# Performance work log

Hardware: AMD Instinct MI355X
Metric: run time of the kernel (lower is better)

The kernel has to match this reference:

```python
import jax, jax.numpy as jnp
import numpy as np

B, T, S, DENC = 32, 256, 1600, 1024
V, EMB, PRE, LSTMU, A, F, K = 1000, 512, 256, 1024, 128, 32, 31


def _lstm_step(x, h, c, W, U, b):
    z = x @ W + h @ U + b
    i, f, g, o = jnp.split(z, 4, axis=-1)
    c2 = jax.nn.sigmoid(f) * c + jax.nn.sigmoid(i) * jnp.tanh(g)
    h2 = jax.nn.sigmoid(o) * jnp.tanh(c2)
    return h2, c2


def setup_inputs() -> dict:
    key = jax.random.key(0)
    ks = jax.random.split(key, 32)
    sc = 0.02
    d = {}
    d['tokens'] = jax.random.randint(ks[0], (B, T), 0, V, dtype=jnp.int32)
    d['memory'] = jax.random.normal(ks[1], (B, S, DENC), dtype=jnp.float32)
    d['memory_length'] = jax.random.randint(ks[2], (B,), S // 2, S, dtype=jnp.int32)
    d['emb'] = sc * jax.random.normal(ks[3], (V, EMB), jnp.float32)
    d['Wp1'] = sc * jax.random.normal(ks[4], (EMB, PRE), jnp.float32)
    d['bp1'] = jnp.zeros((PRE,), jnp.float32)
    d['Wp2'] = sc * jax.random.normal(ks[5], (PRE, PRE), jnp.float32)
    d['bp2'] = jnp.zeros((PRE,), jnp.float32)
    d['Wq'] = sc * jax.random.normal(ks[6], (LSTMU, A), jnp.float32)
    d['Wmem'] = sc * jax.random.normal(ks[7], (DENC, A), jnp.float32)
    d['conv_k'] = sc * jax.random.normal(ks[8], (K, 1, F), jnp.float32)
    d['Wloc'] = sc * jax.random.normal(ks[9], (F, A), jnp.float32)
    d['Wv'] = sc * jax.random.normal(ks[10], (A, 1), jnp.float32)
    d['bv'] = jnp.zeros((1,), jnp.float32)
    d['Wa'] = sc * jax.random.normal(ks[11], (PRE + DENC, 4 * LSTMU), jnp.float32)
    d['Ua'] = sc * jax.random.normal(ks[12], (LSTMU, 4 * LSTMU), jnp.float32)
    d['ba'] = jnp.zeros((4 * LSTMU,), jnp.float32)
    d['W0'] = sc * jax.random.normal(ks[13], (LSTMU + DENC, 4 * LSTMU), jnp.float32)
    d['U0'] = sc * jax.random.normal(ks[14], (LSTMU, 4 * LSTMU), jnp.float32)
    d['b0'] = jnp.zeros((4 * LSTMU,), jnp.float32)
    d['W1'] = sc * jax.random.normal(ks[15], (LSTMU, 4 * LSTMU), jnp.float32)
    d['U1'] = sc * jax.random.normal(ks[16], (LSTMU, 4 * LSTMU), jnp.float32)
    d['b1'] = jnp.zeros((4 * LSTMU,), jnp.float32)
    d['Wc'] = sc * jax.random.normal(ks[17], (LSTMU + DENC, V), jnp.float32)
    d['bc'] = jnp.zeros((V,), jnp.float32)
    d['Ws'] = sc * jax.random.normal(ks[18], (LSTMU + V, 1), jnp.float32)
    d['bs'] = jnp.zeros((1,), jnp.float32)
    return d


def reference(tokens, memory, memory_length, emb, Wp1, bp1, Wp2, bp2, Wq, Wmem,
              conv_k, Wloc, Wv, bv, Wa, Ua, ba, W0, U0, b0, W1, U1, b1,
              Wc, bc, Ws, bs):
    Sdim = memory.shape[1]
    keys = jnp.einsum('bsd,da->bsa', memory, Wmem)            # [B,S,A], computed once
    mask = jnp.arange(Sdim)[None, :] < memory_length[:, None]  # [B,S]
    neg = jnp.float32(-1e9)

    def step(carry, tok):
        h_a, c_a, h0, c0, h1, c1, ctx, ast = carry
        x = emb[tok]                                           # [B,EMB]
        p = jax.nn.relu(x @ Wp1 + bp1)
        p = jax.nn.relu(p @ Wp2 + bp2)                         # prenet (dropout omitted)
        h_a, c_a = _lstm_step(jnp.concatenate([p, ctx], -1), h_a, c_a, Wa, Ua, ba)
        pq = h_a @ Wq                                          # [B,A]
        f = jax.lax.conv_general_dilated(ast[:, :, None], conv_k, (1,), 'SAME',
                                         dimension_numbers=('NWC', 'WIO', 'NWC'))  # [B,S,F]
        ploc = f @ Wloc                                        # [B,S,A]
        e = jnp.squeeze(jnp.tanh(keys + pq[:, None, :] + ploc) @ Wv, -1) + bv  # [B,S]
        e = jnp.where(mask, e, neg)
        al = jax.nn.softmax(e, axis=-1)
        ast = ast + al                                         # cumulative alignments
        ctx = jnp.einsum('bs,bsd->bd', al, memory)
        h0, c0 = _lstm_step(jnp.concatenate([h_a, ctx], -1), h0, c0, W0, U0, b0)
        h1, c1 = _lstm_step(h0, h1, c1, W1, U1, b1)
        proj = jnp.concatenate([h1, ctx], -1)
        cls = proj @ Wc + bc                                   # [B,V]
        stp = jnp.concatenate([h1, cls], -1) @ Ws + bs         # [B,1]
        return (h_a, c_a, h0, c0, h1, c1, ctx, ast), (cls, stp)

    Bz = tokens.shape[0]
    z = lambda n: jnp.zeros((Bz, n), jnp.float32)
    init = (z(LSTMU), z(LSTMU), z(LSTMU), z(LSTMU), z(LSTMU), z(LSTMU),
            z(memory.shape[2]), z(Sdim))
    _, (cls, stp) = jax.lax.scan(step, init, tokens.T)         # stacked [T,B,...]
    return jnp.transpose(cls, (1, 0, 2)), jnp.transpose(stp, (1, 0, 2))
```

## Files before the change

### kernel.cpp

```cpp
#include <hip/hip_runtime.h>

#define BB 32
#define TT 256
#define SS 1600
#define DE 1024
#define VV 1000
#define EM 512
#define PR 256
#define LU 1024
#define AA 128
#define FF 32
#define KK 31
#define KSC 32
#define KSTEP 16
#define NBUF 3

typedef __attribute__((ext_vector_type(8))) short short8;
typedef __attribute__((ext_vector_type(4))) float f32x4;

__device__ __forceinline__ float bf2f(ushort u) {
  unsigned int x = ((unsigned int)u) << 16;
  return __builtin_bit_cast(float, x);
}
__device__ __forceinline__ ushort f2bf(float f) {
  unsigned int x = __builtin_bit_cast(unsigned int, f);
  return (ushort)((x + 0x7FFFu + ((x >> 16) & 1u)) >> 16);
}
__device__ __forceinline__ void gload16(const void* g, void* l) {
  __builtin_amdgcn_global_load_lds(
      (const __attribute__((address_space(1))) void*)g,
      (__attribute__((address_space(3))) void*)l, 16, 0, 0);
}
__device__ __forceinline__ float ftanh(float x) {
  float e = __expf(2.f * x);
  return 1.f - 2.f / (e + 1.f);
}
__device__ __forceinline__ float fsig(float x) {
  return 1.f / (1.f + __expf(-x));
}


__global__ __launch_bounds__(256) void conv_mem(const float* __restrict__ in,
                                                ushort* __restrict__ out, int n4)
{
  int i = blockIdx.x * 256 + threadIdx.x;
  if (i < n4) {
    float4 v = *(const float4*)(in + (size_t)i * 4);
    ushort4 o;
    o.x = f2bf(v.x); o.y = f2bf(v.y); o.z = f2bf(v.z); o.w = f2bf(v.w);
    *(ushort4*)(out + (size_t)i * 4) = o;
  }
}

__global__ __launch_bounds__(256) void pack_wu(const float* __restrict__ Wm,
    const float* __restrict__ Um, int lenW, int ktot, ushort* __restrict__ out, int nS)
{
  int bid = blockIdx.x;
  int kg = bid & 3, S = (bid >> 2) % nS, jb = (bid >> 2) / nS;
  int t = threadIdx.x;
  int c = t >> 1, e4 = (t & 1) * 4;
  int kbase = S * 32 + kg * 8 + e4;
  int j = jb * 128 + c;
  ushort* op = out + ((size_t)(jb * nS + S) * 4 + kg) * 1024 + c * 8 + e4;
#pragma unroll
  for (int i = 0; i < 4; i++) {
    int k = kbase + i;
    float v = 0.f;
    if (k < lenW)      v = Wm[(size_t)k * 4096 + j];
    else if (k < ktot) v = Um[(size_t)(k - lenW) * 4096 + j];
    op[i] = f2bf(v);
  }
}

__global__ __launch_bounds__(256) void keys_kernel(const float* __restrict__ mem,
                                                   const float* __restrict__ Wmem,
                                                   float* __restrict__ keys)
{
  int stile = blockIdx.x;
  int b = blockIdx.y;
  int t = threadIdx.x;
  __shared__ float Xt[8 * 1032];
  const float* mp = mem + ((size_t)b * SS + (size_t)stile * 8) * DE;
  for (int li = t; li < 8 * 256; li += 256) {
    int row = li >> 8, c4 = li & 255;
    float4 v = *(const float4*)(mp + row * DE + c4 * 4);
    *(float4*)(Xt + row * 1032 + c4 * 4) = v;
  }
  __syncthreads();
  int sl = t >> 5, u = t & 31;
  float acc[4] = {0.f, 0.f, 0.f, 0.f};
  for (int k = 0; k < DE; k++) {
    float x = Xt[sl * 1032 + k];
    const float* wr = Wmem + k * AA;
#pragma unroll
    for (int jj = 0; jj < 4; jj++) acc[jj] += x * wr[u + 32 * jj];
  }
  float* kp = keys + ((size_t)b * SS + (size_t)stile * 8 + sl) * AA;
#pragma unroll
  for (int jj = 0; jj < 4; jj++) kp[u + 32 * jj] = acc[jj];
}

__global__ void mconv_kernel(const float* __restrict__ ck, const float* __restrict__ Wloc,
                             float* __restrict__ M)
{
  int a = threadIdx.x;
  int k = blockIdx.x;
  float acc = 0.f;
  for (int c = 0; c < FF; c++) acc += ck[k * FF + c] * Wloc[c * AA + a];
  M[k * AA + a] = acc;
}

__global__ __launch_bounds__(256) void prenet_all(const int* __restrict__ tokens,
    const float* __restrict__ emb, const float* __restrict__ Wp1, const float* __restrict__ bp1,
    const float* __restrict__ Wp2, const float* __restrict__ bp2, float* __restrict__ P)
{
  int tstep = blockIdx.x;
  int bh = blockIdx.y;
  int t = threadIdx.x;
  __shared__ float X[16 * 512];
  __shared__ float P1[16 * 256];
  for (int li = t; li < 16 * 128; li += 256) {
    int bb = li >> 7, c4 = li & 127;
    int tok = tokens[(bh * 16 + bb) * TT + tstep];
    *(float4*)(X + bb * 512 + c4 * 4) = *(const float4*)(emb + (size_t)tok * EM + c4 * 4);
  }
  __syncthreads();
  int j = t;
  float acc[16];
#pragma unroll
  for (int i = 0; i < 16; i++) acc[i] = 0.f;
  for (int k = 0; k < EM; k++) {
    float w = Wp1[k * PR + j];
#pragma unroll
    for (int i = 0; i < 16; i++) acc[i] += X[i * 512 + k] * w;
  }
#pragma unroll
  for (int i = 0; i < 16; i++) P1[i * 256 + j] = fmaxf(acc[i] + bp1[j], 0.f);
  __syncthreads();
#pragma unroll
  for (int i = 0; i < 16; i++) acc[i] = 0.f;
  for (int k = 0; k < PR; k++) {
    float w = Wp2[k * PR + j];
#pragma unroll
    for (int i = 0; i < 16; i++) acc[i] += P1[i * 256 + k] * w;
  }
  float* outp = P + (size_t)tstep * BB * PR + (size_t)bh * 16 * PR;
#pragma unroll
  for (int i = 0; i < 16; i++) outp[i * PR + j] = fmaxf(acc[i] + bp2[j], 0.f);
}


__device__ void gemm_dev(int jb, int kc,
    const float* x0, int len0, const float* x1, int len1, const float* x2, int len2,
    const ushort* WUP, int nS, int chunk, float* zp, char* ldsraw)
{
  ushort* wlT = (ushort*)ldsraw;
  ushort* xl  = (ushort*)(ldsraw + 49152);
  const int t = threadIdx.x;
  const int lane = t & 63;
  const int wv = __builtin_amdgcn_readfirstlane(t >> 6);
  const int PADK = chunk + 8;
  const int nst = chunk >> 6;
  const int k0 = kc * chunk;
  const int S0 = k0 >> 5;
  const size_t jbS = (size_t)jb * nS;
  const int lenW01 = len0 + len1;
  const int ktot = lenW01 + len2;

  auto stage = [&](int s) {
    int buf = s % 3;
    int Sb = S0 + s * 2;
#pragma unroll
    for (int sub = 0; sub < 4; sub++) {
      int inst = wv * 4 + sub;
      const ushort* src = WUP + (jbS + Sb + (inst >> 3)) * 4096
                        + (size_t)(((inst & 7) * 64 + lane) * 8);
      ushort* dst = wlT + buf * 8192 + inst * 512;
      gload16(src, dst);
    }
  };

  stage(0);
  stage(1);

  for (int b = 0; b < 32; b++) {
    for (int kk = t; kk < chunk; kk += 256) {
      int k = k0 + kk;
      float val = 0.f;
      if (k < ktot) {
        const float* xp; int str; int off;
        if (k < len0)        { xp = x0; str = len0; off = k; }
        else if (k < lenW01) { xp = x1; str = len1; off = k - len0; }
        else                 { xp = x2; str = len2; off = k - lenW01; }
        val = xp[(size_t)b * str + off];
      }
      xl[b * PADK + kk] = f2bf(val);
    }
  }
  __syncthreads();

  f32x4 acc[2][2];
#pragma unroll
  for (int mt = 0; mt < 2; mt++)
#pragma unroll
    for (int nt = 0; nt < 2; nt++)
#pragma unroll
      for (int r = 0; r < 4; r++) acc[mt][nt][r] = 0.f;

  const int lane15 = lane & 15, kg = lane >> 4;

  for (int s = 0; s < nst; s++) {
    if (s + 2 < nst) stage(s + 2);
    int ahead = nst - 1 - s; if (ahead > 2) ahead = 2;
    if (ahead == 2)      asm volatile("s_waitcnt vmcnt(8)");
    else if (ahead == 1) asm volatile("s_waitcnt vmcnt(4)");
    else                 asm volatile("s_waitcnt vmcnt(0)");
    __builtin_amdgcn_s_barrier();
    __builtin_amdgcn_sched_barrier(0);
    const ushort* bb = wlT + (s % 3) * 8192 + kg * 1024 + (wv * 32 + lane15) * 8;
    const ushort* ab = xl + lane15 * PADK + s * 64 + kg * 8;
#pragma unroll
    for (int kh = 0; kh < 2; kh++) {
      short8 b0 = *(const short8*)(bb + kh * 4096);
      short8 b1 = *(const short8*)(bb + kh * 4096 + 128);
      short8 a0 = *(const short8*)(ab + kh * 32);
      short8 a1 = *(const short8*)(ab + kh * 32 + 16 * PADK);
      acc[0][0] = __builtin_amdgcn_mfma_f32_16x16x32_bf16(a0, b0, acc[0][0], 0, 0, 0);
      acc[0][1] = __builtin_amdgcn_mfma_f32_16x16x32_bf16(a0, b1, acc[0][1], 0, 0, 0);
      acc[1][0] = __builtin_amdgcn_mfma_f32_16x16x32_bf16(a1, b0, acc[1][0], 0, 0, 0);
      acc[1][1] = __builtin_amdgcn_mfma_f32_16x16x32_bf16(a1, b1, acc[1][1], 0, 0, 0);
    }
    asm volatile("s_waitcnt lgkmcnt(0)");
    __builtin_amdgcn_sched_barrier(0);
    __builtin_amdgcn_s_barrier();
  }

  int colb = jb * 128 + wv * 32 + lane15;
  int rowb = kg * 4;
#pragma unroll
  for (int mt = 0; mt < 2; mt++)
#pragma unroll
    for (int nt = 0; nt < 2; nt++)
#pragma unroll
      for (int r = 0; r < 4; r++) {
        int b = mt * 16 + rowb + r;
        zp[((size_t)kc * BB + b) * 4096 + colb + nt * 16] = acc[mt][nt][r];
      }
}

__device__ void finish_dev(int b, int q, const float* zpart, const float* bias,
    float* h, float* c, const float* Wq, float* pqp, char* ldsraw)
{
  float* sh  = (float*)ldsraw;
  float* sh2 = sh + 256;
  int t = threadIdx.x;
  int j = q * 256 + t;
  float zi = bias[j], zf = bias[LU + j], zg = bias[2 * LU + j], zo = bias[3 * LU + j];
#pragma unroll
  for (int kc = 0; kc < 8; kc++) {
    const float* zpt = zpart + ((size_t)kc * BB + b) * 4096;
    zi += zpt[j]; zf += zpt[LU + j]; zg += zpt[2 * LU + j]; zo += zpt[3 * LU + j];
  }
  float cn = fsig(zf) * c[b * LU + j] + fsig(zi) * ftanh(zg);
  float hn = fsig(zo) * ftanh(cn);
  c[b * LU + j] = cn;
  h[b * LU + j] = hn;

  if (pqp) {
    sh[t] = hn;
    __syncthreads();
    int a = t & 127, half = t >> 7;
    float acc = 0.f;
    const float* wq = Wq + ((size_t)(q * 256 + half * 128)) * AA + a;
#pragma unroll 4
    for (int jj = 0; jj < 128; jj++) acc += sh[half * 128 + jj] * wq[(size_t)jj * AA];
    sh2[t] = acc;
    __syncthreads();
    if (t < 128) pqp[(size_t)q * BB * AA + b * AA + t] = sh2[t] + sh2[t + 128];
  }
}

__device__ void energy_dev(int tile, int b, const float* keys, const float* pqp,
    const float* M, const float* ast, const float* Wv, const float* bv,
    const int* mlen, float* e, char* ldsraw)
{
  int s0 = tile * 128;
  int ml = mlen[b];
  if (s0 >= ml) return;
  float* astT = (float*)ldsraw;
  float* Ml4  = astT + 368;
  float* wvp  = Ml4 + 31 * 132;
  int t = threadIdx.x;
  for (int idx = t; idx < 368; idx += 256) {
    int G = idx >> 3, i = idx & 7;
    int s = s0 + G - 15 + 16 * i;
    astT[idx] = (s >= 0 && s < SS) ? ast[b * SS + s] : 0.f;
  }
  for (int idx = t; idx < KK * AA; idx += 256) {
    int k = idx >> 7, a = idx & 127;
    Ml4[k * 132 + a] = M[idx];
  }
  if (t < 128) wvp[t] = Wv[t];
  else {
    int a = t - 128;
    wvp[128 + a] = pqp[b * AA + a] + pqp[(size_t)BB * AA + b * AA + a]
                 + pqp[(size_t)2 * BB * AA + b * AA + a]
                 + pqp[(size_t)3 * BB * AA + b * AA + a];
  }
  __syncthreads();
  int u = t & 15, g = t >> 4;
  int a0 = u * 8;
  float4 wv0 = *(float4*)&wvp[a0], wv1 = *(float4*)&wvp[a0 + 4];
  float4 pq0 = *(float4*)&wvp[128 + a0], pq1 = *(float4*)&wvp[128 + a0 + 4];
  float arg[8][8];
#pragma unroll
  for (int i = 0; i < 8; i++) {
    int s = s0 + g + 16 * i;
    if (s < SS) {
      const float* kp = keys + ((size_t)b * SS + s) * AA + a0;
      float4 k0 = *(const float4*)kp, k1 = *(const float4*)(kp + 4);
      arg[i][0] = k0.x + pq0.x; arg[i][1] = k0.y + pq0.y;
      arg[i][2] = k0.z + pq0.z; arg[i][3] = k0.w + pq0.w;
      arg[i][4] = k1.x + pq1.x; arg[i][5] = k1.y + pq1.y;
      arg[i][6] = k1.z + pq1.z; arg[i][7] = k1.w + pq1.w;
    } else {
#pragma unroll
      for (int jj = 0; jj < 8; jj++) arg[i][jj] = 0.f;
    }
  }
  for (int k = 0; k < KK; k++) {
    float4 m0 = *(float4*)&Ml4[k * 132 + a0];
    float4 m1 = *(float4*)&Ml4[k * 132 + a0 + 4];
    float4 as0 = *(float4*)&astT[(g + k) * 8];
    float4 as1 = *(float4*)&astT[(g + k) * 8 + 4];
    float asv[8] = {as0.x, as0.y, as0.z, as0.w, as1.x, as1.y, as1.z, as1.w};
#pragma unroll
    for (int i = 0; i < 8; i++) {
      float aw = asv[i];
      arg[i][0] += aw * m0.x; arg[i][1] += aw * m0.y;
      arg[i][2] += aw * m0.z; arg[i][3] += aw * m0.w;
      arg[i][4] += aw * m1.x; arg[i][5] += aw * m1.y;
      arg[i][6] += aw * m1.z; arg[i][7] += aw * m1.w;
    }
  }
  float bvv = bv[0];
#pragma unroll
  for (int i = 0; i < 8; i++) {
    int s = s0 + g + 16 * i;
    float v = ftanh(arg[i][0]) * wv0.x + ftanh(arg[i][1]) * wv0.y
            + ftanh(arg[i][2]) * wv0.z + ftanh(arg[i][3]) * wv0.w
            + ftanh(arg[i][4]) * wv1.x + ftanh(arg[i][5]) * wv1.y
            + ftanh(arg[i][6]) * wv1.z + ftanh(arg[i][7]) * wv1.w;
#pragma unroll
    for (int m = 1; m < 16; m <<= 1) v += __shfl_xor(v, m);
    if (u == 0 && s < SS) e[b * SS + s] = (s < ml) ? (v + bvv) : -1e9f;
  }
}

__device__ void ctxsm_dev(int sc, int b, const float* e, const int* mlen,
    const ushort* mem_bf, float* ast, float* cp, char* ldsraw)
{
  float* red  = (float*)ldsraw;
  float* alsh = red + 4;
  int ml = mlen[b];
  int s0 = sc * 100;
  int cnt = ml - s0; if (cnt > 100) cnt = 100;
  if (cnt <= 0) return;
  int t = threadIdx.x;
  const float* er = e + b * SS;
  float m = -3e38f;
  for (int s = t; s < ml; s += 256) m = fmaxf(m, er[s]);
#pragma unroll
  for (int msk = 1; msk < 64; msk <<= 1) m = fmaxf(m, __shfl_xor(m, msk));
  if ((t & 63) == 0) red[t >> 6] = m;
  __syncthreads();
  m = fmaxf(fmaxf(red[0], red[1]), fmaxf(red[2], red[3]));
  __syncthreads();
  float sum = 0.f;
  for (int s = t; s < ml; s += 256) sum += __expf(er[s] - m);
#pragma unroll
  for (int msk = 1; msk < 64; msk <<= 1) sum += __shfl_xor(sum, msk);
  if ((t & 63) == 0) red[t >> 6] = sum;
  __syncthreads();
  float inv = 1.f / (red[0] + red[1] + red[2] + red[3]);
  if (t < cnt) {
    float a_ = __expf(er[s0 + t] - m) * inv;
    alsh[t] = a_;
    ast[b * SS + s0 + t] += a_;
  }
  __syncthreads();
  float4 acc = make_float4(0.f, 0.f, 0.f, 0.f);
  const ushort* mp = mem_bf + ((size_t)b * SS + s0) * DE + t * 4;
#pragma unroll 4
  for (int i = 0; i < cnt; i++) {
    uint2 v = *(const uint2*)(mp + (size_t)i * DE);
    float a_ = alsh[i];
    acc.x += a_ * bf2f((ushort)(v.x & 0xffff));
    acc.y += a_ * bf2f((ushort)(v.x >> 16));
    acc.z += a_ * bf2f((ushort)(v.y & 0xffff));
    acc.w += a_ * bf2f((ushort)(v.y >> 16));
  }
  *(float4*)&cp[((size_t)sc * BB + b) * DE + t * 4] = acc;
}

__device__ void ctxred_dev(int b, const float* cp, const int* mlen, float* ctx)
{
  int t = threadIdx.x;
  int nsc = (mlen[b] + 99) / 100; if (nsc > 16) nsc = 16;
  float4 acc = make_float4(0.f, 0.f, 0.f, 0.f);
  for (int sc = 0; sc < nsc; sc++) {
    float4 v = *(const float4*)&cp[((size_t)sc * BB + b) * DE + t * 4];
    acc.x += v.x; acc.y += v.y; acc.z += v.z; acc.w += v.w;
  }
  *(float4*)&ctx[b * DE + t * 4] = acc;
}

__device__ void gemv_dev(int jb, int kc,
    const float* x0, int len0, const float* x1, int len1, const float* x2, int len2,
    const float* Wmat, const float* Umat, int N, int chunk, float* zp, char* ldsraw)
{
  float* wl = (float*)ldsraw;
  float* xl = wl + NBUF * KSTEP * 256;
  int t = threadIdx.x;
  int lane = t & 63;
  int wv = __builtin_amdgcn_readfirstlane(t >> 6);
  int lenW = len0 + len1;
  int k0 = kc * chunk;
  int nst = chunk >> 4;
  int colbase = jb * 256 + lane * 4;
  bool jok = (colbase + 4 <= N);

#pragma unroll
  for (int bi = 0; bi < 8; bi++) {
    int b = wv * 8 + bi;
    for (int kk = lane; kk < chunk; kk += 64) {
      int k = k0 + kk;
      const float* xp; int str; int off;
      if (k < len0)      { xp = x0; str = len0; off = k; }
      else if (k < lenW) { xp = x1; str = len1; off = k - len0; }
      else               { xp = x2; str = len2; off = k - lenW; }
      xl[b * 256 + kk] = xp[(size_t)b * str + off];
    }
  }
  __syncthreads();

  auto stage = [&](int s) {
    int buf = s % NBUF;
    int rbase = k0 + s * KSTEP + wv * 4;
#pragma unroll
    for (int rr = 0; rr < 4; rr++) {
      int r = rbase + rr;
      const float* src = (r < lenW) ? (Wmat + (size_t)r * N + colbase)
                                    : (Umat + (size_t)(r - lenW) * N + colbase);
      float* dst = &wl[(buf * KSTEP + (wv * 4 + rr)) * 256];
      if (jok) gload16(src, dst);
    }
  };

  if (nst > 0) stage(0);
  if (nst > 1) stage(1);

  float acc[8][4];
#pragma unroll
  for (int bi = 0; bi < 8; bi++)
    for (int cc = 0; cc < 4; cc++) acc[bi][cc] = 0.f;

  for (int s = 0; s < nst; s++) {
    if (s + 2 < nst) stage(s + 2);
    int ahead = nst - 1 - s; if (ahead > 2) ahead = 2;
    if (ahead == 2)      asm volatile("s_waitcnt vmcnt(8)");
    else if (ahead == 1) asm volatile("s_waitcnt vmcnt(4)");
    else                 asm volatile("s_waitcnt vmcnt(0)");
    __builtin_amdgcn_s_barrier();
    __builtin_amdgcn_sched_barrier(0);
    const float* wb = &wl[(s % NBUF) * KSTEP * 256];
    int xoff = s * KSTEP;
#pragma unroll
    for (int k4 = 0; k4 < 4; k4++) {
      float4 xv[8];
#pragma unroll
      for (int bi = 0; bi < 8; bi++)
        xv[bi] = *(const float4*)&xl[(wv * 8 + bi) * 256 + xoff + k4 * 4];
#pragma unroll
      for (int kk = 0; kk < 4; kk++) {
        float4 w = *(const float4*)&wb[(k4 * 4 + kk) * 256 + lane * 4];
#pragma unroll
        for (int bi = 0; bi < 8; bi++) {
          float xs = (&xv[bi].x)[kk];
          acc[bi][0] += xs * w.x; acc[bi][1] += xs * w.y;
          acc[bi][2] += xs * w.z; acc[bi][3] += xs * w.w;
        }
      }
    }
    asm volatile("s_waitcnt lgkmcnt(0)");
    __builtin_amdgcn_sched_barrier(0);
    __builtin_amdgcn_s_barrier();
  }

  if (jok) {
#pragma unroll
    for (int bi = 0; bi < 8; bi++) {
      int b = wv * 8 + bi;
      *(float4*)&zp[((size_t)kc * BB + b) * N + colbase] =
          make_float4(acc[bi][0], acc[bi][1], acc[bi][2], acc[bi][3]);
    }
  }
}

__device__ void cls_dev(int b, const float* zpc, const float* bc, const float* h1,
                        const float* Ws, const float* bs, float* out, int ts, char* ldsraw)
{
  float* red = (float*)ldsraw;
  int t = threadIdx.x;
  float sacc = 0.f;
  for (int k = t; k < LU; k += 256) sacc += h1[b * LU + k] * Ws[k];
  float* orow = out + (size_t)b * TT * VV + (size_t)ts * VV;
  for (int v = t; v < VV; v += 256) {
    float acc = bc[v];
#pragma unroll
    for (int kc = 0; kc < KSC; kc++) acc += zpc[((size_t)kc * BB + b) * VV + v];
    orow[v] = acc;
    sacc += acc * Ws[LU + v];
  }
#pragma unroll
  for (int msk = 1; msk < 64; msk <<= 1) sacc += __shfl_xor(sacc, msk);
  if ((t & 63) == 0) red[t >> 6] = sacc;
  __syncthreads();
  if (t == 0) out[(size_t)BB * TT * VV + (size_t)b * TT + ts] =
      red[0] + red[1] + red[2] + red[3] + bs[0];
}


__global__ __launch_bounds__(256) void k_gg(
    int nA, const float* ax0, int al0, const float* ax1, int al1,
    const float* ax2, int al2, const ushort* aW, int anS, int achunk, float* azp,
    int nB, const float* bx0, int bl0, const float* bx1, int bl1,
    const float* bx2, int bl2, const ushort* bW, int bnS, int bchunk, float* bzp,
    const float* zpc, const float* bc, const float* h1c,
    const float* Ws, const float* bs, float* out, int ts)
{
  __shared__ alignas(16) char lds[74240];
  int bid = blockIdx.x;
  if (bid < nA + nB) {
    bool fst = bid < nA;
    int l = fst ? bid : bid - nA;
    gemm_dev(l >> 3, l & 7,
             fst ? ax0 : bx0, fst ? al0 : bl0,
             fst ? ax1 : bx1, fst ? al1 : bl1,
             fst ? ax2 : bx2, fst ? al2 : bl2,
             fst ? aW : bW, fst ? anS : bnS, fst ? achunk : bchunk,
             fst ? azp : bzp, lds);
  } else {
    cls_dev(bid - nA - nB, zpc, bc, h1c, Ws, bs, out, ts, lds);
  }
}

__global__ __launch_bounds__(256) void k_ff(
    int n1, const float* z1, const float* bi1, float* h1_, float* c1_,
    const float* Wq1, float* pqp1,
    const float* z2, const float* bi2, float* h2_, float* c2_,
    const float* Wq2, float* pqp2)
{
  __shared__ alignas(16) char lds[4096];
  int bid = blockIdx.x;
  bool fst = bid < n1;
  int l = fst ? bid : bid - n1;
  finish_dev(l >> 2, l & 3,
             fst ? z1 : z2, fst ? bi1 : bi2, fst ? h1_ : h2_, fst ? c1_ : c2_,
             fst ? Wq1 : Wq2, fst ? pqp1 : pqp2, lds);
}

__global__ __launch_bounds__(256) void k_ge(
    int n1, const float* gx0, int gl0, const float* gx1, int gl1,
    const float* gx2, int gl2, const ushort* gW, int gnS, int gchunk, float* gzp,
    const float* keys, const float* pqp, const float* M, const float* ast,
    const float* Wv, const float* bv, const int* mlen, float* e)
{
  __shared__ alignas(16) char lds[74240];
  int bid = blockIdx.x;
  if (bid < n1) {
    gemm_dev(bid >> 3, bid & 7, gx0, gl0, gx1, gl1, gx2, gl2,
             gW, gnS, gchunk, gzp, lds);
  } else {
    int l = bid - n1;
    energy_dev(l / 32, l % 32, keys, pqp, M, ast, Wv, bv, mlen, e, lds);
  }
}

__global__ __launch_bounds__(256) void k_fs(
    int n1, const float* z1, const float* bi1, float* h1_, float* c1_,
    const float* e, const int* mlen, const ushort* membf, float* ast, float* cp)
{
  __shared__ alignas(16) char lds[4096];
  int bid = blockIdx.x;
  if (bid < n1) {
    finish_dev(bid >> 2, bid & 3, z1, bi1, h1_, c1_, nullptr, nullptr, lds);
  } else {
    int l = bid - n1;
    ctxsm_dev(l >> 5, l & 31, e, mlen, membf, ast, cp, lds);
  }
}

__global__ __launch_bounds__(256) void k_gr(
    int n1, const float* vx0, int vl0, const float* vx1, int vl1,
    const float* vx2, int vl2, const float* Wm, const float* Um, int N, int vchunk,
    float* vzp, const float* cp, const int* mlen, float* ctxout)
{
  __shared__ alignas(16) char lds[81920];
  int bid = blockIdx.x;
  if (bid < n1) {
    gemv_dev(bid >> 5, bid & 31, vx0, vl0, vx1, vl1, vx2, vl2,
             Wm, Um, N, vchunk, vzp, lds);
  } else {
    ctxred_dev(bid - n1, cp, mlen, ctxout);
  }
}


extern "C" void kernel_launch(void* const* d_in, const int* in_sizes, int n_in,
                              void* d_out, int out_size, void* d_ws, size_t ws_size,
                              hipStream_t stream)
{
  const int*   tokens = (const int*)  d_in[0];
  const float* memory = (const float*)d_in[1];
  const int*   mlen   = (const int*)  d_in[2];
  const float* emb    = (const float*)d_in[3];
  const float* Wp1    = (const float*)d_in[4];
  const float* bp1    = (const float*)d_in[5];
  const float* Wp2    = (const float*)d_in[6];
  const float* bp2    = (const float*)d_in[7];
  const float* Wq     = (const float*)d_in[8];
  const float* Wmem   = (const float*)d_in[9];
  const float* convk  = (const float*)d_in[10];
  const float* Wloc   = (const float*)d_in[11];
  const float* Wv     = (const float*)d_in[12];
  const float* bv     = (const float*)d_in[13];
  const float* Wa     = (const float*)d_in[14];
  const float* Ua     = (const float*)d_in[15];
  const float* ba     = (const float*)d_in[16];
  const float* W0     = (const float*)d_in[17];
  const float* U0     = (const float*)d_in[18];
  const float* b0     = (const float*)d_in[19];
  const float* W1     = (const float*)d_in[20];
  const float* U1     = (const float*)d_in[21];
  const float* b1     = (const float*)d_in[22];
  const float* Wc     = (const float*)d_in[23];
  const float* bc     = (const float*)d_in[24];
  const float* Ws     = (const float*)d_in[25];
  const float* bs     = (const float*)d_in[26];
  float* out = (float*)d_out;
  float* ws = (float*)d_ws;

  size_t o = 0;
  float* keys  = ws + o;  o += (size_t)BB * SS * AA;
  float* Mv    = ws + o;  o += 4096;
  float* P_all = ws + o;  o += (size_t)TT * BB * PR;
  float* st    = ws + o;
  float* h_a = st;
  float* c_a = h_a + BB * LU;
  float* h0  = c_a + BB * LU;
  float* c0  = h0 + BB * LU;
  float* h1  = c0 + BB * LU;
  float* c1  = h1 + BB * LU;
  float* ctx2 = c1 + BB * LU;
  float* ast = ctx2 + 2 * BB * DE;
  size_t stcount = (size_t)6 * BB * LU + (size_t)2 * BB * DE + (size_t)BB * SS;
  o += stcount;
  float* pqp  = ws + o;  o += (size_t)4 * BB * AA;
  float* ebuf = ws + o;  o += (size_t)BB * SS;
  float* zpA  = ws + o;  o += (size_t)8 * BB * 4096;
  float* zp0  = ws + o;  o += (size_t)8 * BB * 4096;
  float* zp1  = ws + o;  o += (size_t)8 * BB * 4096;
  float* zpc  = ws + o;  o += (size_t)KSC * BB * VV;
  float* cp   = ws + o;  o += (size_t)16 * BB * DE;
  ushort* membf = (ushort*)(ws + o);  o += (size_t)BB * SS * DE / 2;
  ushort* WUPa  = (ushort*)(ws + o);  o += (size_t)2560 * 4096 / 2;
  ushort* WUP0  = (ushort*)(ws + o);  o += (size_t)3072 * 4096 / 2;
  ushort* WUP1  = (ushort*)(ws + o);  o += (size_t)2048 * 4096 / 2;

  hipMemsetAsync(st, 0, stcount * sizeof(float), stream);
  conv_mem<<<(BB * SS * DE / 4 + 255) / 256, 256, 0, stream>>>(memory, membf,
                                                               BB * SS * DE / 4);
  pack_wu<<<32 * 80 * 4, 256, 0, stream>>>(Wa, Ua, PR + DE, 2304, WUPa, 80);
  pack_wu<<<32 * 96 * 4, 256, 0, stream>>>(W0, U0, LU + DE, 3072, WUP0, 96);
  pack_wu<<<32 * 64 * 4, 256, 0, stream>>>(W1, U1, LU, 2048, WUP1, 64);
  keys_kernel<<<dim3(200, BB), 256, 0, stream>>>(memory, Wmem, keys);
  mconv_kernel<<<KK, AA, 0, stream>>>(convk, Wloc, Mv);
  prenet_all<<<dim3(TT, 2), 256, 0, stream>>>(tokens, emb, Wp1, bp1, Wp2, bp2, P_all);

  auto ctx_at = [&](int t) { return ctx2 + (size_t)(t & 1) * BB * DE; };

  k_gg<<<256, 256, 0, stream>>>(
      0, P_all, PR, ctx_at(1), DE, h_a, LU, WUPa, 80, 320, zpA,
      256, P_all, PR, ctx_at(1), DE, h_a, LU, WUPa, 80, 320, zpA,
      zpc, bc, h1, Ws, bs, out, 0);
  k_ff<<<128, 256, 0, stream>>>(
      128, zpA, ba, h_a, c_a, Wq, pqp,
      zpA, ba, h_a, c_a, Wq, pqp);
  k_ge<<<416, 256, 0, stream>>>(
      0, h_a, LU, ctx_at(0), DE, h0, LU, WUP0, 96, 384, zp0,
      keys, pqp, Mv, ast, Wv, bv, mlen, ebuf);
  k_fs<<<512, 256, 0, stream>>>(
      0, zp0, b0, h0, c0,
      ebuf, mlen, membf, ast, cp);
  k_gr<<<32, 256, 0, stream>>>(
      0, h1, LU, ctx_at(0), DE, h1, 0, Wc, Wc, VV, 64, zpc,
      cp, mlen, ctx_at(0));

  for (int t = 0; t < TT - 1; t++) {
    int ncls = (t > 0) ? 32 : 0;
    k_gg<<<512 + ncls, 256, 0, stream>>>(
        256, h_a, LU, ctx_at(t), DE, h0, LU, WUP0, 96, 384, zp0,
        256, P_all + (size_t)(t + 1) * BB * PR, PR, ctx_at(t), DE, h_a, LU,
        WUPa, 80, 320, zpA,
        zpc, bc, h1, Ws, bs, out, t - 1);
    k_ff<<<256, 256, 0, stream>>>(
        128, zp0, b0, h0, c0, nullptr, nullptr,
        zpA, ba, h_a, c_a, Wq, pqp);
    k_ge<<<672, 256, 0, stream>>>(
        256, h0, LU, h1, LU, h0, 0, WUP1, 64, 256, zp1,
        keys, pqp, Mv, ast, Wv, bv, mlen, ebuf);
    k_fs<<<640, 256, 0, stream>>>(
        128, zp1, b1, h1, c1,
        ebuf, mlen, membf, ast, cp);
    k_gr<<<160, 256, 0, stream>>>(
        128, h1, LU, ctx_at(t), DE, h1, 0, Wc, Wc, VV, 64, zpc,
        cp, mlen, ctx_at(t + 1));
  }

  {
    int t = TT - 1;
    k_gg<<<256 + 32, 256, 0, stream>>>(
        256, h_a, LU, ctx_at(t), DE, h0, LU, WUP0, 96, 384, zp0,
        0, P_all, PR, ctx_at(t), DE, h_a, LU, WUPa, 80, 320, zpA,
        zpc, bc, h1, Ws, bs, out, t - 1);
    k_ff<<<128, 256, 0, stream>>>(
        128, zp0, b0, h0, c0, nullptr, nullptr,
        zp0, b0, h0, c0, nullptr, nullptr);
    k_ge<<<256, 256, 0, stream>>>(
        256, h0, LU, h1, LU, h0, 0, WUP1, 64, 256, zp1,
        keys, pqp, Mv, ast, Wv, bv, mlen, ebuf);
    k_fs<<<128, 256, 0, stream>>>(
        128, zp1, b1, h1, c1,
        ebuf, mlen, membf, ast, cp);
    k_gr<<<128, 256, 0, stream>>>(
        128, h1, LU, ctx_at(t), DE, h1, 0, Wc, Wc, VV, 64, zpc,
        cp, mlen, ctx_at(t + 1));
    k_gg<<<32, 256, 0, stream>>>(
        0, h_a, LU, ctx_at(t), DE, h0, LU, WUP0, 96, 384, zp0,
        0, P_all, PR, ctx_at(t), DE, h_a, LU, WUPa, 80, 320, zpA,
        zpc, bc, h1, Ws, bs, out, t);
  }
}
```

Before: 27.42 ms.

## Reduce per-step kernel launches by atomic context reduction and restaged pipeline

The per-timestep schedule is restructured from five kernels into four. The context partial-sum buffer and its separate reduction pass are replaced by atomicAdd accumulation into a context buffer that a co-scheduled block zeroes in advance. The classifier GEMV is deferred one step and fused into the LSTM-finish kernel, and the classifier/stop output is fused into the energy kernel. The GEMV pipeline also drops from triple to double buffering. The goal is to cut launch and serialization overhead in the 256-step recurrence, at the cost of atomic contention, non-deterministic summation order, and a shallower prefetch depth.

```diff
diff --git a/kernel.cpp b/kernel.cpp
--- a/kernel.cpp
+++ b/kernel.cpp
@@ -357,14 +357,14 @@
   }
 }
 
-__device__ void ctxsm_dev(int sc, int b, const float* e, const int* mlen,
-    const ushort* mem_bf, float* ast, float* cp, char* ldsraw)
+__device__ void ctxsm_atomic_dev(int sc, int b, const float* e, const int* mlen,
+    const ushort* mem_bf, float* ast, float* ctx, char* ldsraw)
 {
   float* red  = (float*)ldsraw;
   float* alsh = red + 4;
   int ml = mlen[b];
-  int s0 = sc * 100;
-  int cnt = ml - s0; if (cnt > 100) cnt = 100;
+  int s0 = sc * 200;
+  int cnt = ml - s0; if (cnt > 200) cnt = 200;
   if (cnt <= 0) return;
   int t = threadIdx.x;
   const float* er = e + b * SS;
@@ -400,27 +400,19 @@
     acc.z += a_ * bf2f((ushort)(v.y & 0xffff));
     acc.w += a_ * bf2f((ushort)(v.y >> 16));
   }
-  *(float4*)&cp[((size_t)sc * BB + b) * DE + t * 4] = acc;
-}
-
-__device__ void ctxred_dev(int b, const float* cp, const int* mlen, float* ctx)
-{
-  int t = threadIdx.x;
-  int nsc = (mlen[b] + 99) / 100; if (nsc > 16) nsc = 16;
-  float4 acc = make_float4(0.f, 0.f, 0.f, 0.f);
-  for (int sc = 0; sc < nsc; sc++) {
-    float4 v = *(const float4*)&cp[((size_t)sc * BB + b) * DE + t * 4];
-    acc.x += v.x; acc.y += v.y; acc.z += v.z; acc.w += v.w;
-  }
-  *(float4*)&ctx[b * DE + t * 4] = acc;
-}
-
-__device__ void gemv_dev(int jb, int kc,
+  float* cpx = ctx + b * DE + t * 4;
+  atomicAdd(cpx + 0, acc.x);
+  atomicAdd(cpx + 1, acc.y);
+  atomicAdd(cpx + 2, acc.z);
+  atomicAdd(cpx + 3, acc.w);
+}
+
+__device__ void gemv2_dev(int jb, int kc,
     const float* x0, int len0, const float* x1, int len1, const float* x2, int len2,
     const float* Wmat, const float* Umat, int N, int chunk, float* zp, char* ldsraw)
 {
   float* wl = (float*)ldsraw;
-  float* xl = wl + NBUF * KSTEP * 256;
+  float* xl = wl + 2 * KSTEP * 256;
   int t = threadIdx.x;
   int lane = t & 63;
   int wv = __builtin_amdgcn_readfirstlane(t >> 6);
@@ -445,7 +437,7 @@
   __syncthreads();
 
   auto stage = [&](int s) {
-    int buf = s % NBUF;
+    int buf = s & 1;
     int rbase = k0 + s * KSTEP + wv * 4;
 #pragma unroll
     for (int rr = 0; rr < 4; rr++) {
@@ -458,7 +450,6 @@
   };
 
   if (nst > 0) stage(0);
-  if (nst > 1) stage(1);
 
   float acc[8][4];
 #pragma unroll
@@ -466,14 +457,11 @@
     for (int cc = 0; cc < 4; cc++) acc[bi][cc] = 0.f;
 
   for (int s = 0; s < nst; s++) {
-    if (s + 2 < nst) stage(s + 2);
-    int ahead = nst - 1 - s; if (ahead > 2) ahead = 2;
-    if (ahead == 2)      asm volatile("s_waitcnt vmcnt(8)");
-    else if (ahead == 1) asm volatile("s_waitcnt vmcnt(4)");
-    else                 asm volatile("s_waitcnt vmcnt(0)");
+    if (s + 1 < nst) { stage(s + 1); asm volatile("s_waitcnt vmcnt(4)"); }
+    else             { asm volatile("s_waitcnt vmcnt(0)"); }
     __builtin_amdgcn_s_barrier();
     __builtin_amdgcn_sched_barrier(0);
-    const float* wb = &wl[(s % NBUF) * KSTEP * 256];
+    const float* wb = &wl[(s & 1) * KSTEP * 256];
     int xoff = s * KSTEP;
 #pragma unroll
     for (int k4 = 0; k4 < 4; k4++) {
@@ -535,84 +523,79 @@
     int nA, const float* ax0, int al0, const float* ax1, int al1,
     const float* ax2, int al2, const ushort* aW, int anS, int achunk, float* azp,
     int nB, const float* bx0, int bl0, const float* bx1, int bl1,
-    const float* bx2, int bl2, const ushort* bW, int bnS, int bchunk, float* bzp,
-    const float* zpc, const float* bc, const float* h1c,
-    const float* Ws, const float* bs, float* out, int ts)
+    const float* bx2, int bl2, const ushort* bW, int bnS, int bchunk, float* bzp)
 {
   __shared__ alignas(16) char lds[74240];
   int bid = blockIdx.x;
-  if (bid < nA + nB) {
-    bool fst = bid < nA;
-    int l = fst ? bid : bid - nA;
-    gemm_dev(l >> 3, l & 7,
-             fst ? ax0 : bx0, fst ? al0 : bl0,
-             fst ? ax1 : bx1, fst ? al1 : bl1,
-             fst ? ax2 : bx2, fst ? al2 : bl2,
-             fst ? aW : bW, fst ? anS : bnS, fst ? achunk : bchunk,
-             fst ? azp : bzp, lds);
+  bool fst = bid < nA;
+  int l = fst ? bid : bid - nA;
+  gemm_dev(l >> 3, l & 7,
+           fst ? ax0 : bx0, fst ? al0 : bl0,
+           fst ? ax1 : bx1, fst ? al1 : bl1,
+           fst ? ax2 : bx2, fst ? al2 : bl2,
+           fst ? aW : bW, fst ? anS : bnS, fst ? achunk : bchunk,
+           fst ? azp : bzp, lds);
+}
+
+__global__ __launch_bounds__(256) void k_ffg(
+    int nf0, const float* z0, const float* bi0, float* h0p, float* c0p,
+    int nf1, const float* z1, const float* bi1, float* h1p, float* c1p,
+    const float* Wq, float* pqp,
+    int ng, const float* vx0, int vl0, const float* vx1, int vl1,
+    const float* vx2, int vl2, const float* Wm, const float* Um, int N, int vchunk,
+    float* vzp)
+{
+  __shared__ alignas(16) char lds[65536];
+  int bid = blockIdx.x;
+  if (bid < nf0) {
+    finish_dev(bid >> 2, bid & 3, z0, bi0, h0p, c0p, nullptr, nullptr, lds);
+  } else if (bid < nf0 + nf1) {
+    int l = bid - nf0;
+    finish_dev(l >> 2, l & 3, z1, bi1, h1p, c1p, Wq, pqp, lds);
   } else {
-    cls_dev(bid - nA - nB, zpc, bc, h1c, Ws, bs, out, ts, lds);
-  }
-}
-
-__global__ __launch_bounds__(256) void k_ff(
-    int n1, const float* z1, const float* bi1, float* h1_, float* c1_,
-    const float* Wq1, float* pqp1,
-    const float* z2, const float* bi2, float* h2_, float* c2_,
-    const float* Wq2, float* pqp2)
-{
-  __shared__ alignas(16) char lds[4096];
-  int bid = blockIdx.x;
-  bool fst = bid < n1;
-  int l = fst ? bid : bid - n1;
-  finish_dev(l >> 2, l & 3,
-             fst ? z1 : z2, fst ? bi1 : bi2, fst ? h1_ : h2_, fst ? c1_ : c2_,
-             fst ? Wq1 : Wq2, fst ? pqp1 : pqp2, lds);
-}
-
-__global__ __launch_bounds__(256) void k_ge(
-    int n1, const float* gx0, int gl0, const float* gx1, int gl1,
+    int l = bid - nf0 - nf1;
+    gemv2_dev(l >> 5, l & 31, vx0, vl0, vx1, vl1, vx2, vl2,
+              Wm, Um, N, vchunk, vzp, lds);
+  }
+}
+
+__global__ __launch_bounds__(256) void k_gec(
+    int nG, const float* gx0, int gl0, const float* gx1, int gl1,
     const float* gx2, int gl2, const ushort* gW, int gnS, int gchunk, float* gzp,
-    const float* keys, const float* pqp, const float* M, const float* ast,
-    const float* Wv, const float* bv, const int* mlen, float* e)
+    int nE, const float* keys, const float* pqp, const float* M, const float* ast,
+    const float* Wv, const float* bv, const int* mlen, float* e,
+    int nC, const float* zpc, const float* bc, const float* h1c,
+    const float* Ws, const float* bs, float* out, int ts,
+    int nZ, float* zctx)
 {
   __shared__ alignas(16) char lds[74240];
   int bid = blockIdx.x;
-  if (bid < n1) {
+  if (bid < nG) {
     gemm_dev(bid >> 3, bid & 7, gx0, gl0, gx1, gl1, gx2, gl2,
              gW, gnS, gchunk, gzp, lds);
+  } else if (bid < nG + nE) {
+    int l = bid - nG;
+    energy_dev(l / 32, l % 32, keys, pqp, M, ast, Wv, bv, mlen, e, lds);
+  } else if (bid < nG + nE + nC) {
+    cls_dev(bid - nG - nE, zpc, bc, h1c, Ws, bs, out, ts, lds);
   } else {
-    int l = bid - n1;
-    energy_dev(l / 32, l % 32, keys, pqp, M, ast, Wv, bv, mlen, e, lds);
-  }
-}
-
-__global__ __launch_bounds__(256) void k_fs(
-    int n1, const float* z1, const float* bi1, float* h1_, float* c1_,
-    const float* e, const int* mlen, const ushort* membf, float* ast, float* cp)
-{
-  __shared__ alignas(16) char lds[4096];
+    int b = bid - nG - nE - nC;
+    *(float4*)&zctx[b * DE + threadIdx.x * 4] = make_float4(0.f, 0.f, 0.f, 0.f);
+  }
+}
+
+__global__ __launch_bounds__(256) void k_fsa(
+    int nF, const float* z1, const float* bi1, float* h1p, float* c1p,
+    int nS, const float* e, const int* mlen, const ushort* membf,
+    float* ast, float* ctx)
+{
+  __shared__ alignas(16) char lds[8192];
   int bid = blockIdx.x;
-  if (bid < n1) {
-    finish_dev(bid >> 2, bid & 3, z1, bi1, h1_, c1_, nullptr, nullptr, lds);
+  if (bid < nF) {
+    finish_dev(bid >> 2, bid & 3, z1, bi1, h1p, c1p, nullptr, nullptr, lds);
   } else {
-    int l = bid - n1;
-    ctxsm_dev(l >> 5, l & 31, e, mlen, membf, ast, cp, lds);
-  }
-}
-
-__global__ __launch_bounds__(256) void k_gr(
-    int n1, const float* vx0, int vl0, const float* vx1, int vl1,
-    const float* vx2, int vl2, const float* Wm, const float* Um, int N, int vchunk,
-    float* vzp, const float* cp, const int* mlen, float* ctxout)
-{
-  __shared__ alignas(16) char lds[81920];
-  int bid = blockIdx.x;
-  if (bid < n1) {
-    gemv_dev(bid >> 5, bid & 31, vx0, vl0, vx1, vl1, vx2, vl2,
-             Wm, Um, N, vchunk, vzp, lds);
-  } else {
-    ctxred_dev(bid - n1, cp, mlen, ctxout);
+    int l = bid - nF;
+    ctxsm_atomic_dev(l >> 5, l & 31, e, mlen, membf, ast, ctx, lds);
   }
 }
 
@@ -672,7 +655,6 @@
   float* zp0  = ws + o;  o += (size_t)8 * BB * 4096;
   float* zp1  = ws + o;  o += (size_t)8 * BB * 4096;
   float* zpc  = ws + o;  o += (size_t)KSC * BB * VV;
-  float* cp   = ws + o;  o += (size_t)16 * BB * DE;
   ushort* membf = (ushort*)(ws + o);  o += (size_t)BB * SS * DE / 2;
   ushort* WUPa  = (ushort*)(ws + o);  o += (size_t)2560 * 4096 / 2;
   ushort* WUP0  = (ushort*)(ws + o);  o += (size_t)3072 * 4096 / 2;
@@ -691,64 +673,67 @@
   auto ctx_at = [&](int t) { return ctx2 + (size_t)(t & 1) * BB * DE; };
 
   k_gg<<<256, 256, 0, stream>>>(
-      0, P_all, PR, ctx_at(1), DE, h_a, LU, WUPa, 80, 320, zpA,
-      256, P_all, PR, ctx_at(1), DE, h_a, LU, WUPa, 80, 320, zpA,
-      zpc, bc, h1, Ws, bs, out, 0);
-  k_ff<<<128, 256, 0, stream>>>(
+      0, P_all, PR, ctx2 + BB * DE, DE, h_a, LU, WUPa, 80, 320, zpA,
+      256, P_all, PR, ctx2 + BB * DE, DE, h_a, LU, WUPa, 80, 320, zpA);
+  k_ffg<<<128, 256, 0, stream>>>(
+      0, zpA, ba, h_a, c_a,
       128, zpA, ba, h_a, c_a, Wq, pqp,
-      zpA, ba, h_a, c_a, Wq, pqp);
-  k_ge<<<416, 256, 0, stream>>>(
-      0, h_a, LU, ctx_at(0), DE, h0, LU, WUP0, 96, 384, zp0,
-      keys, pqp, Mv, ast, Wv, bv, mlen, ebuf);
-  k_fs<<<512, 256, 0, stream>>>(
-      0, zp0, b0, h0, c0,
-      ebuf, mlen, membf, ast, cp);
-  k_gr<<<32, 256, 0, stream>>>(
-      0, h1, LU, ctx_at(0), DE, h1, 0, Wc, Wc, VV, 64, zpc,
-      cp, mlen, ctx_at(0));
-
-  for (int t = 0; t < TT - 1; t++) {
-    int ncls = (t > 0) ? 32 : 0;
-    k_gg<<<512 + ncls, 256, 0, stream>>>(
-        256, h_a, LU, ctx_at(t), DE, h0, LU, WUP0, 96, 384, zp0,
-        256, P_all + (size_t)(t + 1) * BB * PR, PR, ctx_at(t), DE, h_a, LU,
-        WUPa, 80, 320, zpA,
-        zpc, bc, h1, Ws, bs, out, t - 1);
-    k_ff<<<256, 256, 0, stream>>>(
-        128, zp0, b0, h0, c0, nullptr, nullptr,
-        zpA, ba, h_a, c_a, Wq, pqp);
-    k_ge<<<672, 256, 0, stream>>>(
+      0, h1, LU, ctx2, DE, h1, 0, Wc, Wc, VV, 64, zpc);
+  k_gec<<<416, 256, 0, stream>>>(
+      0, h_a, LU, ctx2, DE, h0, LU, WUP0, 96, 384, zp0,
+      416, keys, pqp, Mv, ast, Wv, bv, mlen, ebuf,
+      0, zpc, bc, h1, Ws, bs, out, 0,
+      0, ctx2);
+  k_fsa<<<256, 256, 0, stream>>>(
+      0, zp1, b1, h1, c1,
+      256, ebuf, mlen, membf, ast, ctx_at(0));
+
+  for (int i = 0; i < TT - 1; i++) {
+    int ng  = (i > 0) ? 128 : 0;
+    int ncl = (i > 0) ? 32 : 0;
+    k_gg<<<512, 256, 0, stream>>>(
+        256, h_a, LU, ctx_at(i), DE, h0, LU, WUP0, 96, 384, zp0,
+        256, P_all + (size_t)(i + 1) * BB * PR, PR, ctx_at(i), DE, h_a, LU,
+        WUPa, 80, 320, zpA);
+    k_ffg<<<256 + ng, 256, 0, stream>>>(
+        128, zp0, b0, h0, c0,
+        128, zpA, ba, h_a, c_a, Wq, pqp,
+        ng, h1, LU, ctx_at(i - 1), DE, h1, 0, Wc, Wc, VV, 64, zpc);
+    k_gec<<<256 + 416 + ncl + 32, 256, 0, stream>>>(
         256, h0, LU, h1, LU, h0, 0, WUP1, 64, 256, zp1,
-        keys, pqp, Mv, ast, Wv, bv, mlen, ebuf);
-    k_fs<<<640, 256, 0, stream>>>(
+        416, keys, pqp, Mv, ast, Wv, bv, mlen, ebuf,
+        ncl, zpc, bc, h1, Ws, bs, out, i - 1,
+        32, ctx_at(i + 1));
+    k_fsa<<<384, 256, 0, stream>>>(
         128, zp1, b1, h1, c1,
-        ebuf, mlen, membf, ast, cp);
-    k_gr<<<160, 256, 0, stream>>>(
-        128, h1, LU, ctx_at(t), DE, h1, 0, Wc, Wc, VV, 64, zpc,
-        cp, mlen, ctx_at(t + 1));
+        256, ebuf, mlen, membf, ast, ctx_at(i + 1));
   }
 
   {
-    int t = TT - 1;
-    k_gg<<<256 + 32, 256, 0, stream>>>(
-        256, h_a, LU, ctx_at(t), DE, h0, LU, WUP0, 96, 384, zp0,
-        0, P_all, PR, ctx_at(t), DE, h_a, LU, WUPa, 80, 320, zpA,
-        zpc, bc, h1, Ws, bs, out, t - 1);
-    k_ff<<<128, 256, 0, stream>>>(
-        128, zp0, b0, h0, c0, nullptr, nullptr,
-        zp0, b0, h0, c0, nullptr, nullptr);
-    k_ge<<<256, 256, 0, stream>>>(
+    int i = TT - 1;
+    k_gg<<<256, 256, 0, stream>>>(
+        256, h_a, LU, ctx_at(i), DE, h0, LU, WUP0, 96, 384, zp0,
+        0, P_all, PR, ctx_at(i), DE, h_a, LU, WUPa, 80, 320, zpA);
+    k_ffg<<<256, 256, 0, stream>>>(
+        128, zp0, b0, h0, c0,
+        0, zpA, ba, h_a, c_a, Wq, pqp,
+        128, h1, LU, ctx_at(i - 1), DE, h1, 0, Wc, Wc, VV, 64, zpc);
+    k_gec<<<256 + 32, 256, 0, stream>>>(
         256, h0, LU, h1, LU, h0, 0, WUP1, 64, 256, zp1,
-        keys, pqp, Mv, ast, Wv, bv, mlen, ebuf);
-    k_fs<<<128, 256, 0, stream>>>(
+        0, keys, pqp, Mv, ast, Wv, bv, mlen, ebuf,
+        32, zpc, bc, h1, Ws, bs, out, i - 1,
+        0, ctx_at(i + 1));
+    k_fsa<<<128, 256, 0, stream>>>(
         128, zp1, b1, h1, c1,
-        ebuf, mlen, membf, ast, cp);
-    k_gr<<<128, 256, 0, stream>>>(
-        128, h1, LU, ctx_at(t), DE, h1, 0, Wc, Wc, VV, 64, zpc,
-        cp, mlen, ctx_at(t + 1));
-    k_gg<<<32, 256, 0, stream>>>(
-        0, h_a, LU, ctx_at(t), DE, h0, LU, WUP0, 96, 384, zp0,
-        0, P_all, PR, ctx_at(t), DE, h_a, LU, WUPa, 80, 320, zpA,
-        zpc, bc, h1, Ws, bs, out, t);
-  }
-}
+        0, ebuf, mlen, membf, ast, ctx_at(i + 1));
+    k_ffg<<<128, 256, 0, stream>>>(
+        0, zp0, b0, h0, c0,
+        0, zpA, ba, h_a, c_a, Wq, pqp,
+        128, h1, LU, ctx_at(i), DE, h1, 0, Wc, Wc, VV, 64, zpc);
+    k_gec<<<32, 256, 0, stream>>>(
+        0, h0, LU, h1, LU, h0, 0, WUP1, 64, 256, zp1,
+        0, keys, pqp, Mv, ast, Wv, bv, mlen, ebuf,
+        32, zpc, bc, h1, Ws, bs, out, i,
+        0, ctx_at(i + 1));
+  }
+}
```

New measurement: 25.54 ms. 1.07x faster.
